# Kernel optimization log

Measured on AMD Instinct MI355X. Metric: run time of the kernel, lower is better.

Reference implementation:

```python
import jax, jax.numpy as jnp
import numpy as np

B, S, D, O, C = 4, 2048, 1024, 1024, 8


def setup_inputs() -> dict:
    key = jax.random.key(0)
    k1, k2, k3, k4 = jax.random.split(key, 4)
    x = jax.random.normal(k1, (B, S, D), dtype=jnp.float32)
    category_id = jax.random.randint(k2, (B, S), 0, C, dtype=jnp.int64)
    weight = jax.random.normal(k3, (C, D, O), dtype=jnp.float32)
    bias = jax.random.normal(k4, (C, O), dtype=jnp.float32)
    return {"x": x, "category_id": category_id, "weight": weight, "bias": bias}


def reference(x, category_id, weight, bias):
    # Faithful to: out[t] = x[t] @ weight[cid[t]] + bias[cid[t]]
    # Instead of gathering a full [T, D, O] weight tensor per token (32GB),
    # compute every category's projection once and select per token.
    orig_shape = x.shape
    x_flat = x.reshape(-1, orig_shape[-1])          # [T, D]
    cid = category_id.reshape(-1)                    # [T]
    out_all = jnp.einsum('td,cdo->tco', x_flat, weight)  # [T, C, O]
    out = jnp.take_along_axis(out_all, cid[:, None, None], axis=1)[:, 0, :]  # [T, O]
    out = out + bias[cid]
    return out.reshape(orig_shape[:-1] + (weight.shape[-1],))
```

## Files before the change

### kernel.cpp

```cpp
#include <hip/hip_runtime.h>

#define TOK   8192
#define DIM   1024
#define OUTD  1024
#define NCAT  8
#define BM    128
#define BN    128
#define BK    32
#define NKT   (DIM / BK)
#define MAX_MT 71
#define MPMAX (MAX_MT * BM)

typedef __attribute__((ext_vector_type(8))) __bf16 bf16x8;
typedef __attribute__((ext_vector_type(4))) float  f32x4;

__device__ __forceinline__ unsigned short f2bf(float f) {
  unsigned u = __float_as_uint(f);
  u += 0x7fffu + ((u >> 16) & 1u);
  return (unsigned short)(u >> 16);
}

__global__ __launch_bounds__(256) void k_prep(const float* __restrict__ w,
    const int* __restrict__ cid, unsigned short* __restrict__ wt,
    int* __restrict__ row_token, int* __restrict__ tile_c, int* __restrict__ tile_m) {
  int tid = threadIdx.x;
  if (blockIdx.x < 2048) {
    int b = blockIdx.x;
    int ot = b & 15, dt = (b >> 4) & 15, c = b >> 8;
    __shared__ unsigned short t[64][72];
    int i  = tid >> 2;
    int jg = tid & 3;
    const float* src = w + ((size_t)c << 20) + (size_t)(dt * 64 + i) * 1024 + ot * 64 + jg * 16;
    #pragma unroll
    for (int q = 0; q < 4; ++q) {
      float4 v = *(const float4*)(src + q * 4);
      t[jg * 16 + q * 4 + 0][i] = f2bf(v.x);
      t[jg * 16 + q * 4 + 1][i] = f2bf(v.y);
      t[jg * 16 + q * 4 + 2][i] = f2bf(v.z);
      t[jg * 16 + q * 4 + 3][i] = f2bf(v.w);
    }
    __syncthreads();
    unsigned short* dst = wt + ((size_t)c << 20) + (size_t)(ot * 64 + i) * 1024 + dt * 64 + jg * 16;
    uint4 a = *(const uint4*)&t[i][jg * 16];
    uint4 bq = *(const uint4*)&t[i][jg * 16 + 8];
    *(uint4*)dst = a;
    *(uint4*)(dst + 8) = bq;
    return;
  }

  __shared__ int wcnt[4][NCAT];
  __shared__ int wbase[4][NCAT];
  __shared__ int gbase[NCAT];
  int lane = tid & 63, wave = tid >> 6;
  int base = wave * 2048;

  int cs[32];
  #pragma unroll
  for (int it = 0; it < 32; ++it) cs[it] = cid[base + it * 64 + lane];
  int cnt_loc[NCAT];
  #pragma unroll
  for (int c = 0; c < NCAT; ++c) cnt_loc[c] = 0;
  #pragma unroll
  for (int it = 0; it < 32; ++it)
    #pragma unroll
    for (int c = 0; c < NCAT; ++c)
      cnt_loc[c] += __popcll(__ballot(cs[it] == c));
  if (lane == 0) {
    #pragma unroll
    for (int c = 0; c < NCAT; ++c) wcnt[wave][c] = cnt_loc[c];
  }
  __syncthreads();

  if (tid == 0) {
    int pr = 0, mt = 0;
    for (int c = 0; c < NCAT; ++c) {
      int tot = 0;
      for (int wv = 0; wv < 4; ++wv) { wbase[wv][c] = tot; tot += wcnt[wv][c]; }
      gbase[c] = pr;
      int nt = (tot + BM - 1) / BM;
      for (int i = 0; i < nt; ++i) { tile_c[mt] = c; tile_m[mt] = pr + i * BM; ++mt; }
      pr += nt * BM;
    }
    for (; mt < MAX_MT; ++mt) { tile_c[mt] = -1; tile_m[mt] = 0; }
  }
  __syncthreads();
  for (int r = tid; r < MPMAX; r += 256) row_token[r] = -1;
  __syncthreads();

  int run[NCAT];
  #pragma unroll
  for (int c = 0; c < NCAT; ++c) run[c] = gbase[c] + wbase[wave][c];
  unsigned long long lt = (lane == 63) ? ~0ull >> 1 : ((1ull << lane) - 1);
  #pragma unroll
  for (int it = 0; it < 32; ++it) {
    int c = cs[it];
    int pos = 0;
    #pragma unroll
    for (int cat = 0; cat < NCAT; ++cat) {
      unsigned long long m = __ballot(cs[it] == cat);
      if (cat == c) pos = run[cat] + __popcll(m & lt);
      run[cat] += __popcll(m);
    }
    row_token[pos] = base + it * 64 + lane;
  }
}

__global__ __launch_bounds__(256) void k_gemm(const float* __restrict__ x,
    const unsigned short* __restrict__ wt, const float* __restrict__ bias,
    const int* __restrict__ row_token, const int* __restrict__ tile_c,
    const int* __restrict__ tile_m, float* __restrict__ out) {
  int wg  = blockIdx.x;
  int lin = (wg & 7) * MAX_MT + (wg >> 3);
  int mt  = lin >> 3;
  int nt  = lin & 7;
  int c = tile_c[mt];
  if (c < 0) return;
  int m0 = tile_m[mt];
  int n0 = nt * BN;

  __shared__ unsigned short As[2][BM][BK];
  __shared__ unsigned short Bs[2][BM][BK];

  int tid  = threadIdx.x;
  int lane = tid & 63;
  int wr = (tid >> 6) >> 1, wc = (tid >> 6) & 1;

  f32x4 acc[4][4];
  #pragma unroll
  for (int m = 0; m < 4; ++m)
    #pragma unroll
    for (int n = 0; n < 4; ++n) acc[m][n] = (f32x4){0.f, 0.f, 0.f, 0.f};

  int arowS = tid >> 1;
  int khalf = (tid & 1) << 4;
  int tk = row_token[m0 + arowS];
  bool avalid = tk >= 0;
  const float* xs = x + (size_t)(avalid ? tk : 0) * DIM + khalf;
  int g0   = (tid & 1) << 1;
  int aswz = (arowS >> 1) & 3;
  int a0 = ((g0 ^ aswz) << 3);
  int a1 = (((g0 + 1) ^ aswz) << 3);

  int srow = tid >> 2;
  int sdst = (tid & 3) << 3;
  int gsrc = (((tid & 3) ^ ((tid >> 3) & 3)) << 3);
  const unsigned short* Bg = wt + ((size_t)c << 20) + (size_t)n0 * DIM;

  float4 v0, v1, v2, v3;
  auto LOADA = [&](int kt) {
    v0 = *(const float4*)(xs + kt);
    v1 = *(const float4*)(xs + kt + 4);
    v2 = *(const float4*)(xs + kt + 8);
    v3 = *(const float4*)(xs + kt + 12);
  };
  auto WRITEA = [&](int b) {
    bf16x8 p0, p1;
    p0[0] = (__bf16)v0.x; p0[1] = (__bf16)v0.y; p0[2] = (__bf16)v0.z; p0[3] = (__bf16)v0.w;
    p0[4] = (__bf16)v1.x; p0[5] = (__bf16)v1.y; p0[6] = (__bf16)v1.z; p0[7] = (__bf16)v1.w;
    p1[0] = (__bf16)v2.x; p1[1] = (__bf16)v2.y; p1[2] = (__bf16)v2.z; p1[3] = (__bf16)v2.w;
    p1[4] = (__bf16)v3.x; p1[5] = (__bf16)v3.y; p1[6] = (__bf16)v3.z; p1[7] = (__bf16)v3.w;
    if (!avalid) { p0 = (bf16x8){}; p1 = (bf16x8){}; }
    *(bf16x8*)&As[b][arowS][a0] = p0;
    *(bf16x8*)&As[b][arowS][a1] = p1;
  };
  auto STAGEB = [&](int b, int kt) {
    __builtin_amdgcn_global_load_lds(
      (const __attribute__((address_space(1))) unsigned int*)(Bg + (size_t)srow * DIM + kt + gsrc),
      (__attribute__((address_space(3))) unsigned int*)(&Bs[b][srow][sdst]), 16, 0, 0);
    __builtin_amdgcn_global_load_lds(
      (const __attribute__((address_space(1))) unsigned int*)(Bg + (size_t)(srow + 64) * DIM + kt + gsrc),
      (__attribute__((address_space(3))) unsigned int*)(&Bs[b][srow + 64][sdst]), 16, 0, 0);
  };

  int rcol = (((lane >> 4) ^ (((lane & 15) >> 1) & 3)) << 3);
  int arow = wr * 64 + (lane & 15);
  int brow = wc * 64 + (lane & 15);

  LOADA(0);
  STAGEB(0, 0);
  WRITEA(0);
  __syncthreads();

  int cur = 0;
  for (int t = 0; t < NKT; ++t) {
    bool pre = (t + 1 < NKT);
    if (pre) { LOADA((t + 1) * BK); STAGEB(cur ^ 1, (t + 1) * BK); }

    bf16x8 af[4], bf[4];
    #pragma unroll
    for (int m = 0; m < 4; ++m)
      af[m] = *(const bf16x8*)&As[cur][arow + m * 16][rcol];
    #pragma unroll
    for (int n = 0; n < 4; ++n)
      bf[n] = *(const bf16x8*)&Bs[cur][brow + n * 16][rcol];
    #pragma unroll
    for (int m = 0; m < 4; ++m)
      #pragma unroll
      for (int n = 0; n < 4; ++n)
        acc[m][n] = __builtin_amdgcn_mfma_f32_16x16x32_bf16(af[m], bf[n], acc[m][n], 0, 0, 0);

    if (pre) WRITEA(cur ^ 1);
    __syncthreads();
    cur ^= 1;
  }

  int col = lane & 15;
  int rq  = (lane >> 4) << 2;
  float bv[4];
  #pragma unroll
  for (int n = 0; n < 4; ++n) bv[n] = bias[c * OUTD + n0 + wc * 64 + n * 16 + col];
  #pragma unroll
  for (int m = 0; m < 4; ++m) {
    #pragma unroll
    for (int r = 0; r < 4; ++r) {
      int prow = m0 + wr * 64 + m * 16 + rq + r;
      int tok = row_token[prow];
      if (tok < 0) continue;
      float* orow = out + (size_t)tok * OUTD + n0 + wc * 64 + col;
      #pragma unroll
      for (int n = 0; n < 4; ++n) orow[n * 16] = acc[m][n][r] + bv[n];
    }
  }
}

extern "C" void kernel_launch(void* const* d_in, const int* in_sizes, int n_in,
                              void* d_out, int out_size, void* d_ws, size_t ws_size,
                              hipStream_t stream) {
  const float* x    = (const float*)d_in[0];
  const int*   cid  = (const int*)d_in[1];
  const float* w    = (const float*)d_in[2];
  const float* bias = (const float*)d_in[3];
  float* out = (float*)d_out;

  char* ws = (char*)d_ws;
  constexpr size_t WT_BYTES = (size_t)NCAT * DIM * OUTD * 2;
  constexpr size_t RT_BYTES = (size_t)MPMAX * 4;
  unsigned short* wtb = (unsigned short*)ws;
  int* row_token = (int*)(ws + WT_BYTES);
  int* tile_c    = (int*)(ws + WT_BYTES + RT_BYTES);
  int* tile_m    = tile_c + MAX_MT;

  k_prep<<<2049, 256, 0, stream>>>(w, cid, wtb, row_token, tile_c, tile_m);
  k_gemm<<<8 * MAX_MT, 256, 0, stream>>>(x, wtb, bias, row_token, tile_c, tile_m, out);
}
```

Measured before the change: 177.9 us.

## Pre-gather bf16 activations and restructure GEMM pipeline with 8 waves, BK=64

Adds a separate gather kernel that converts the routed token rows of x to bf16 into a contiguous workspace, so the GEMM can stage both A and B with direct global-to-LDS loads instead of register loads and conversions. The GEMM moves to 512 threads (8 waves of 64x32 sub-tiles), doubles BK to 64, and splits each k-step into two halves with staggered A/B staging, explicit waitcnt/barriers and setprio around the MFMA blocks. This is meant to cut VGPR pressure and A-conversion latency in the main loop. In exchange it adds an extra kernel launch, a roughly 18 MB bf16 round-trip through memory, and more barriers per iteration.

```diff
diff --git a/kernel.cpp b/kernel.cpp
--- a/kernel.cpp
+++ b/kernel.cpp
@@ -6,13 +6,16 @@
 #define NCAT  8
 #define BM    128
 #define BN    128
-#define BK    32
+#define BK    64
 #define NKT   (DIM / BK)
 #define MAX_MT 71
 #define MPMAX (MAX_MT * BM)
 
 typedef __attribute__((ext_vector_type(8))) __bf16 bf16x8;
 typedef __attribute__((ext_vector_type(4))) float  f32x4;
+
+#define GLP(p)  (const __attribute__((address_space(1))) unsigned int*)(p)
+#define LDSP(p) (__attribute__((address_space(3))) unsigned int*)(p)
 
 __device__ __forceinline__ unsigned short f2bf(float f) {
   unsigned u = __float_as_uint(f);
@@ -105,7 +108,26 @@
   }
 }
 
-__global__ __launch_bounds__(256) void k_gemm(const float* __restrict__ x,
+__global__ __launch_bounds__(256) void k_gather(const float* __restrict__ x,
+    const int* __restrict__ row_token, unsigned short* __restrict__ xg) {
+  int idx = blockIdx.x * 256 + threadIdx.x;
+  int r  = idx >> 7;
+  int e0 = (idx & 127) << 3;
+  if (r >= MPMAX) return;
+  int tok = row_token[r];
+  union { unsigned short u[8]; uint4 v; } o;
+  if (tok >= 0) {
+    const float4* s = (const float4*)(x + (size_t)tok * DIM + e0);
+    float4 a = s[0], b = s[1];
+    o.u[0] = f2bf(a.x); o.u[1] = f2bf(a.y); o.u[2] = f2bf(a.z); o.u[3] = f2bf(a.w);
+    o.u[4] = f2bf(b.x); o.u[5] = f2bf(b.y); o.u[6] = f2bf(b.z); o.u[7] = f2bf(b.w);
+  } else {
+    o.v = make_uint4(0u, 0u, 0u, 0u);
+  }
+  *(uint4*)(xg + (size_t)r * DIM + e0) = o.v;
+}
+
+__global__ __launch_bounds__(512, 4) void k_gemm(const unsigned short* __restrict__ xg,
     const unsigned short* __restrict__ wt, const float* __restrict__ bias,
     const int* __restrict__ row_token, const int* __restrict__ tile_c,
     const int* __restrict__ tile_m, float* __restrict__ out) {
@@ -123,92 +145,101 @@
 
   int tid  = threadIdx.x;
   int lane = tid & 63;
-  int wr = (tid >> 6) >> 1, wc = (tid >> 6) & 1;
-
-  f32x4 acc[4][4];
+  int wave = tid >> 6;
+  int wr = wave >> 2, wc = wave & 3;
+
+  f32x4 acc[4][2];
   #pragma unroll
   for (int m = 0; m < 4; ++m)
     #pragma unroll
-    for (int n = 0; n < 4; ++n) acc[m][n] = (f32x4){0.f, 0.f, 0.f, 0.f};
-
-  int arowS = tid >> 1;
-  int khalf = (tid & 1) << 4;
-  int tk = row_token[m0 + arowS];
-  bool avalid = tk >= 0;
-  const float* xs = x + (size_t)(avalid ? tk : 0) * DIM + khalf;
-  int g0   = (tid & 1) << 1;
-  int aswz = (arowS >> 1) & 3;
-  int a0 = ((g0 ^ aswz) << 3);
-  int a1 = (((g0 + 1) ^ aswz) << 3);
-
-  int srow = tid >> 2;
-  int sdst = (tid & 3) << 3;
-  int gsrc = (((tid & 3) ^ ((tid >> 3) & 3)) << 3);
+    for (int n = 0; n < 2; ++n) acc[m][n] = (f32x4){0.f, 0.f, 0.f, 0.f};
+
+  const unsigned short* Ag = xg + (size_t)m0 * DIM;
   const unsigned short* Bg = wt + ((size_t)c << 20) + (size_t)n0 * DIM;
 
-  float4 v0, v1, v2, v3;
-  auto LOADA = [&](int kt) {
-    v0 = *(const float4*)(xs + kt);
-    v1 = *(const float4*)(xs + kt + 4);
-    v2 = *(const float4*)(xs + kt + 8);
-    v3 = *(const float4*)(xs + kt + 12);
+  int row0 = tid >> 3,         gp0 = tid & 7;
+  int row1 = (512 + tid) >> 3, gp1 = tid & 7;
+  int gl0 = (gp0 ^ (row0 & 7)) << 3;
+  int gl1 = (gp1 ^ (row1 & 7)) << 3;
+
+  auto STAGE_A = [&](int b, int kt) {
+    __builtin_amdgcn_global_load_lds(GLP(Ag + (size_t)row0 * DIM + kt + gl0),
+                                     LDSP(&As[b][row0][gp0 << 3]), 16, 0, 0);
+    __builtin_amdgcn_global_load_lds(GLP(Ag + (size_t)row1 * DIM + kt + gl1),
+                                     LDSP(&As[b][row1][gp1 << 3]), 16, 0, 0);
   };
-  auto WRITEA = [&](int b) {
-    bf16x8 p0, p1;
-    p0[0] = (__bf16)v0.x; p0[1] = (__bf16)v0.y; p0[2] = (__bf16)v0.z; p0[3] = (__bf16)v0.w;
-    p0[4] = (__bf16)v1.x; p0[5] = (__bf16)v1.y; p0[6] = (__bf16)v1.z; p0[7] = (__bf16)v1.w;
-    p1[0] = (__bf16)v2.x; p1[1] = (__bf16)v2.y; p1[2] = (__bf16)v2.z; p1[3] = (__bf16)v2.w;
-    p1[4] = (__bf16)v3.x; p1[5] = (__bf16)v3.y; p1[6] = (__bf16)v3.z; p1[7] = (__bf16)v3.w;
-    if (!avalid) { p0 = (bf16x8){}; p1 = (bf16x8){}; }
-    *(bf16x8*)&As[b][arowS][a0] = p0;
-    *(bf16x8*)&As[b][arowS][a1] = p1;
+  auto STAGE_B = [&](int b, int kt) {
+    __builtin_amdgcn_global_load_lds(GLP(Bg + (size_t)row0 * DIM + kt + gl0),
+                                     LDSP(&Bs[b][row0][gp0 << 3]), 16, 0, 0);
+    __builtin_amdgcn_global_load_lds(GLP(Bg + (size_t)row1 * DIM + kt + gl1),
+                                     LDSP(&Bs[b][row1][gp1 << 3]), 16, 0, 0);
   };
-  auto STAGEB = [&](int b, int kt) {
-    __builtin_amdgcn_global_load_lds(
-      (const __attribute__((address_space(1))) unsigned int*)(Bg + (size_t)srow * DIM + kt + gsrc),
-      (__attribute__((address_space(3))) unsigned int*)(&Bs[b][srow][sdst]), 16, 0, 0);
-    __builtin_amdgcn_global_load_lds(
-      (const __attribute__((address_space(1))) unsigned int*)(Bg + (size_t)(srow + 64) * DIM + kt + gsrc),
-      (__attribute__((address_space(3))) unsigned int*)(&Bs[b][srow + 64][sdst]), 16, 0, 0);
-  };
-
-  int rcol = (((lane >> 4) ^ (((lane & 15) >> 1) & 3)) << 3);
-  int arow = wr * 64 + (lane & 15);
-  int brow = wc * 64 + (lane & 15);
-
-  LOADA(0);
-  STAGEB(0, 0);
-  WRITEA(0);
-  __syncthreads();
+
+  int lr = lane & 15, lq = lane >> 4, l7 = lane & 7;
+  int goff0 = ((0 + lq) ^ l7) << 3;
+  int goff1 = ((4 + lq) ^ l7) << 3;
+  int arow = wr * 64 + lr;
+  int brow = wc * 32 + lr;
+
+  STAGE_A(0, 0);
+  STAGE_B(0, 0);
 
   int cur = 0;
   for (int t = 0; t < NKT; ++t) {
+    int ktn = (t + 1) * BK;
     bool pre = (t + 1 < NKT);
-    if (pre) { LOADA((t + 1) * BK); STAGEB(cur ^ 1, (t + 1) * BK); }
-
-    bf16x8 af[4], bf[4];
-    #pragma unroll
-    for (int m = 0; m < 4; ++m)
-      af[m] = *(const bf16x8*)&As[cur][arow + m * 16][rcol];
-    #pragma unroll
-    for (int n = 0; n < 4; ++n)
-      bf[n] = *(const bf16x8*)&Bs[cur][brow + n * 16][rcol];
-    #pragma unroll
-    for (int m = 0; m < 4; ++m)
-      #pragma unroll
-      for (int n = 0; n < 4; ++n)
-        acc[m][n] = __builtin_amdgcn_mfma_f32_16x16x32_bf16(af[m], bf[n], acc[m][n], 0, 0, 0);
-
-    if (pre) WRITEA(cur ^ 1);
-    __syncthreads();
+
+    if (pre) STAGE_A(cur ^ 1, ktn);
+    if (pre) asm volatile("s_waitcnt vmcnt(2)" ::: "memory");
+    else     asm volatile("s_waitcnt vmcnt(0)" ::: "memory");
+    __builtin_amdgcn_s_barrier();
+
+    {
+      bf16x8 af[4], bf[2];
+      #pragma unroll
+      for (int m = 0; m < 4; ++m)
+        af[m] = *(const bf16x8*)&As[cur][arow + m * 16][goff0];
+      #pragma unroll
+      for (int n = 0; n < 2; ++n)
+        bf[n] = *(const bf16x8*)&Bs[cur][brow + n * 16][goff0];
+      __builtin_amdgcn_s_setprio(1);
+      #pragma unroll
+      for (int m = 0; m < 4; ++m)
+        #pragma unroll
+        for (int n = 0; n < 2; ++n)
+          acc[m][n] = __builtin_amdgcn_mfma_f32_16x16x32_bf16(af[m], bf[n], acc[m][n], 0, 0, 0);
+      __builtin_amdgcn_s_setprio(0);
+    }
+    asm volatile("s_waitcnt lgkmcnt(0)" ::: "memory");
+    __builtin_amdgcn_s_barrier();
+
+    if (pre) STAGE_B(cur ^ 1, ktn);
+    {
+      bf16x8 af[4], bf[2];
+      #pragma unroll
+      for (int m = 0; m < 4; ++m)
+        af[m] = *(const bf16x8*)&As[cur][arow + m * 16][goff1];
+      #pragma unroll
+      for (int n = 0; n < 2; ++n)
+        bf[n] = *(const bf16x8*)&Bs[cur][brow + n * 16][goff1];
+      __builtin_amdgcn_s_setprio(1);
+      #pragma unroll
+      for (int m = 0; m < 4; ++m)
+        #pragma unroll
+        for (int n = 0; n < 2; ++n)
+          acc[m][n] = __builtin_amdgcn_mfma_f32_16x16x32_bf16(af[m], bf[n], acc[m][n], 0, 0, 0);
+      __builtin_amdgcn_s_setprio(0);
+    }
+    asm volatile("s_waitcnt lgkmcnt(0)" ::: "memory");
+    __builtin_amdgcn_s_barrier();
     cur ^= 1;
   }
 
-  int col = lane & 15;
-  int rq  = (lane >> 4) << 2;
-  float bv[4];
-  #pragma unroll
-  for (int n = 0; n < 4; ++n) bv[n] = bias[c * OUTD + n0 + wc * 64 + n * 16 + col];
+  int col = lr;
+  int rq  = lq << 2;
+  float bv[2];
+  #pragma unroll
+  for (int n = 0; n < 2; ++n) bv[n] = bias[c * OUTD + n0 + wc * 32 + n * 16 + col];
   #pragma unroll
   for (int m = 0; m < 4; ++m) {
     #pragma unroll
@@ -216,9 +247,9 @@
       int prow = m0 + wr * 64 + m * 16 + rq + r;
       int tok = row_token[prow];
       if (tok < 0) continue;
-      float* orow = out + (size_t)tok * OUTD + n0 + wc * 64 + col;
-      #pragma unroll
-      for (int n = 0; n < 4; ++n) orow[n * 16] = acc[m][n][r] + bv[n];
+      float* orow = out + (size_t)tok * OUTD + n0 + wc * 32 + col;
+      #pragma unroll
+      for (int n = 0; n < 2; ++n) orow[n * 16] = acc[m][n][r] + bv[n];
     }
   }
 }
@@ -233,13 +264,16 @@
   float* out = (float*)d_out;
 
   char* ws = (char*)d_ws;
+  constexpr size_t XG_BYTES = (size_t)MPMAX * DIM * 2;
   constexpr size_t WT_BYTES = (size_t)NCAT * DIM * OUTD * 2;
   constexpr size_t RT_BYTES = (size_t)MPMAX * 4;
-  unsigned short* wtb = (unsigned short*)ws;
-  int* row_token = (int*)(ws + WT_BYTES);
-  int* tile_c    = (int*)(ws + WT_BYTES + RT_BYTES);
+  unsigned short* xg  = (unsigned short*)ws;
+  unsigned short* wtb = (unsigned short*)(ws + XG_BYTES);
+  int* row_token = (int*)(ws + XG_BYTES + WT_BYTES);
+  int* tile_c    = (int*)(ws + XG_BYTES + WT_BYTES + RT_BYTES);
   int* tile_m    = tile_c + MAX_MT;
 
   k_prep<<<2049, 256, 0, stream>>>(w, cid, wtb, row_token, tile_c, tile_m);
-  k_gemm<<<8 * MAX_MT, 256, 0, stream>>>(x, wtb, bias, row_token, tile_c, tile_m, out);
-}
+  k_gather<<<(MPMAX * (DIM / 8) + 255) / 256, 256, 0, stream>>>(x, row_token, xg);
+  k_gemm<<<8 * MAX_MT, 512, 0, stream>>>(xg, wtb, bias, row_token, tile_c, tile_m, out);
+}
```

New measurement: 164.4 us. -7.6%, faster.

## Triple-buffer GEMM k-loop with two-stage-ahead prefetch and explicit waitcnts

Applied to the files above, without the earlier changes.

Moves the grouped GEMM main loop from double to triple LDS buffering. The B tile (global_load_lds) and the A registers for tile t+2 are issued while tile t is computed. Manual s_waitcnt vmcnt(6) and lgkmcnt plus raw s_barrier replace __syncthreads so two tiles of loads can stay in flight. The goal is to hide global memory latency better, at the cost of more LDS use, more registers for two A staging sets, and fragile hand-counted wait counts.

```diff
diff --git a/kernel.cpp b/kernel.cpp
--- a/kernel.cpp
+++ b/kernel.cpp
@@ -13,6 +13,9 @@
 
 typedef __attribute__((ext_vector_type(8))) __bf16 bf16x8;
 typedef __attribute__((ext_vector_type(4))) float  f32x4;
+
+#define GLP(p)  (const __attribute__((address_space(1))) unsigned int*)(p)
+#define LDSP(p) (__attribute__((address_space(3))) unsigned int*)(p)
 
 __device__ __forceinline__ unsigned short f2bf(float f) {
   unsigned u = __float_as_uint(f);
@@ -118,8 +121,8 @@
   int m0 = tile_m[mt];
   int n0 = nt * BN;
 
-  __shared__ unsigned short As[2][BM][BK];
-  __shared__ unsigned short Bs[2][BM][BK];
+  __shared__ unsigned short As[3][BM][BK];
+  __shared__ unsigned short Bs[3][BM][BK];
 
   int tid  = threadIdx.x;
   int lane = tid & 63;
@@ -131,77 +134,85 @@
     #pragma unroll
     for (int n = 0; n < 4; ++n) acc[m][n] = (f32x4){0.f, 0.f, 0.f, 0.f};
 
-  int arowS = tid >> 1;
-  int khalf = (tid & 1) << 4;
-  int tk = row_token[m0 + arowS];
-  bool avalid = tk >= 0;
-  const float* xs = x + (size_t)(avalid ? tk : 0) * DIM + khalf;
-  int g0   = (tid & 1) << 1;
-  int aswz = (arowS >> 1) & 3;
-  int a0 = ((g0 ^ aswz) << 3);
-  int a1 = (((g0 + 1) ^ aswz) << 3);
+  int ra = tid >> 1;
+  int kh = (tid & 1) << 4;
+  int tokA = row_token[m0 + ra];
+  const float* xs = x + (size_t)(tokA < 0 ? 0 : tokA) * DIM + kh;
+  int aw = (ra >> 1) & 3;
+  int g0 = (tid & 1) << 1;
+  int a0 = ((g0 ^ aw) << 3);
+  int a1 = (((g0 + 1) ^ aw) << 3);
 
   int srow = tid >> 2;
   int sdst = (tid & 3) << 3;
   int gsrc = (((tid & 3) ^ ((tid >> 3) & 3)) << 3);
   const unsigned short* Bg = wt + ((size_t)c << 20) + (size_t)n0 * DIM;
 
-  float4 v0, v1, v2, v3;
-  auto LOADA = [&](int kt) {
-    v0 = *(const float4*)(xs + kt);
-    v1 = *(const float4*)(xs + kt + 4);
-    v2 = *(const float4*)(xs + kt + 8);
-    v3 = *(const float4*)(xs + kt + 12);
-  };
-  auto WRITEA = [&](int b) {
+  auto STAGE_B = [&](int b, int kt) {
+    __builtin_amdgcn_global_load_lds(GLP(Bg + (size_t)srow * DIM + kt + gsrc),
+                                     LDSP(&Bs[b][srow][sdst]), 16, 0, 0);
+    __builtin_amdgcn_global_load_lds(GLP(Bg + (size_t)(srow + 64) * DIM + kt + gsrc),
+                                     LDSP(&Bs[b][srow + 64][sdst]), 16, 0, 0);
+  };
+
+  float4 sA0[4], sA1[4];
+  auto AISSUE = [&](float4 (&s)[4], int t) {
+    const float* p = xs + t * BK;
+    #pragma unroll
+    for (int q = 0; q < 4; ++q) s[q] = *(const float4*)(p + 4 * q);
+  };
+  auto AWRITE = [&](float4 (&s)[4], int b) {
     bf16x8 p0, p1;
-    p0[0] = (__bf16)v0.x; p0[1] = (__bf16)v0.y; p0[2] = (__bf16)v0.z; p0[3] = (__bf16)v0.w;
-    p0[4] = (__bf16)v1.x; p0[5] = (__bf16)v1.y; p0[6] = (__bf16)v1.z; p0[7] = (__bf16)v1.w;
-    p1[0] = (__bf16)v2.x; p1[1] = (__bf16)v2.y; p1[2] = (__bf16)v2.z; p1[3] = (__bf16)v2.w;
-    p1[4] = (__bf16)v3.x; p1[5] = (__bf16)v3.y; p1[6] = (__bf16)v3.z; p1[7] = (__bf16)v3.w;
-    if (!avalid) { p0 = (bf16x8){}; p1 = (bf16x8){}; }
-    *(bf16x8*)&As[b][arowS][a0] = p0;
-    *(bf16x8*)&As[b][arowS][a1] = p1;
-  };
-  auto STAGEB = [&](int b, int kt) {
-    __builtin_amdgcn_global_load_lds(
-      (const __attribute__((address_space(1))) unsigned int*)(Bg + (size_t)srow * DIM + kt + gsrc),
-      (__attribute__((address_space(3))) unsigned int*)(&Bs[b][srow][sdst]), 16, 0, 0);
-    __builtin_amdgcn_global_load_lds(
-      (const __attribute__((address_space(1))) unsigned int*)(Bg + (size_t)(srow + 64) * DIM + kt + gsrc),
-      (__attribute__((address_space(3))) unsigned int*)(&Bs[b][srow + 64][sdst]), 16, 0, 0);
+    p0[0] = (__bf16)s[0].x; p0[1] = (__bf16)s[0].y; p0[2] = (__bf16)s[0].z; p0[3] = (__bf16)s[0].w;
+    p0[4] = (__bf16)s[1].x; p0[5] = (__bf16)s[1].y; p0[6] = (__bf16)s[1].z; p0[7] = (__bf16)s[1].w;
+    p1[0] = (__bf16)s[2].x; p1[1] = (__bf16)s[2].y; p1[2] = (__bf16)s[2].z; p1[3] = (__bf16)s[2].w;
+    p1[4] = (__bf16)s[3].x; p1[5] = (__bf16)s[3].y; p1[6] = (__bf16)s[3].z; p1[7] = (__bf16)s[3].w;
+    if (tokA < 0) { p0 = (bf16x8){}; p1 = (bf16x8){}; }
+    *(bf16x8*)&As[b][ra][a0] = p0;
+    *(bf16x8*)&As[b][ra][a1] = p1;
   };
 
   int rcol = (((lane >> 4) ^ (((lane & 15) >> 1) & 3)) << 3);
   int arow = wr * 64 + (lane & 15);
   int brow = wc * 64 + (lane & 15);
 
-  LOADA(0);
-  STAGEB(0, 0);
-  WRITEA(0);
-  __syncthreads();
-
-  int cur = 0;
-  for (int t = 0; t < NKT; ++t) {
-    bool pre = (t + 1 < NKT);
-    if (pre) { LOADA((t + 1) * BK); STAGEB(cur ^ 1, (t + 1) * BK); }
-
+  STAGE_B(0, 0);      AISSUE(sA0, 0);
+  STAGE_B(1, BK);     AISSUE(sA1, 1);
+  asm volatile("s_waitcnt vmcnt(6)" ::: "memory");
+  AWRITE(sA0, 0);
+  asm volatile("s_waitcnt lgkmcnt(0)" ::: "memory");
+  __builtin_amdgcn_s_barrier();
+
+  auto BODY = [&](int t, float4 (&sI)[4], float4 (&sW)[4]) {
+    bool pre2 = (t + 2 < NKT);
+    bool pre1 = (t + 1 < NKT);
+    if (pre2) { STAGE_B((t + 2) % 3, (t + 2) * BK); AISSUE(sI, t + 2); }
+
+    int b = t % 3;
     bf16x8 af[4], bf[4];
     #pragma unroll
     for (int m = 0; m < 4; ++m)
-      af[m] = *(const bf16x8*)&As[cur][arow + m * 16][rcol];
+      af[m] = *(const bf16x8*)&As[b][arow + m * 16][rcol];
     #pragma unroll
     for (int n = 0; n < 4; ++n)
-      bf[n] = *(const bf16x8*)&Bs[cur][brow + n * 16][rcol];
+      bf[n] = *(const bf16x8*)&Bs[b][brow + n * 16][rcol];
     #pragma unroll
     for (int m = 0; m < 4; ++m)
       #pragma unroll
       for (int n = 0; n < 4; ++n)
         acc[m][n] = __builtin_amdgcn_mfma_f32_16x16x32_bf16(af[m], bf[n], acc[m][n], 0, 0, 0);
 
-    if (pre) WRITEA(cur ^ 1);
-    __syncthreads();
-    cur ^= 1;
+    if (pre1) {
+      if (pre2) asm volatile("s_waitcnt vmcnt(6)" ::: "memory");
+      else      asm volatile("s_waitcnt vmcnt(0)" ::: "memory");
+      AWRITE(sW, (t + 1) % 3);
+      asm volatile("s_waitcnt lgkmcnt(0)" ::: "memory");
+      __builtin_amdgcn_s_barrier();
+    }
+  };
+  for (int t2 = 0; t2 < NKT; t2 += 2) {
+    BODY(t2,     sA0, sA1);
+    BODY(t2 + 1, sA1, sA0);
   }
 
   int col = lane & 15;
```

New measurement: 180.5 us. About the same (+1.5%).
